# Performance work log

Measured on AMD Instinct MI355X. Metric: run time of the kernel, lower is better.

The kernel has to match this reference:

```python
import jax, jax.numpy as jnp
import numpy as np

BN_EPS = 1e-5


def setup_inputs() -> dict:
    key = jax.random.key(0)
    ks = jax.random.split(key, 10)
    D, N, NDRUG, NTAIL, NREL = 256, 128, 572, 100000, 100
    return {
        "drug_table": jax.random.normal(ks[0], (NDRUG, D), jnp.float32),
        "rela_table": jax.random.normal(ks[1], (NREL, D), jnp.float32),
        "ent_table": jax.random.normal(ks[2], (NTAIL, D), jnp.float32),
        "W1": jax.random.normal(ks[3], (NDRUG, D, D), jnp.float32),
        "b1": jax.random.normal(ks[4], (N, D), jnp.float32),
        "W2": jax.random.normal(ks[5], (NDRUG, D, D), jnp.float32),
        "b2": jax.random.normal(ks[6], (N, D), jnp.float32),
        "lin_w": jax.random.normal(ks[7], (D, 2 * D), jnp.float32) * (1.0 / np.sqrt(2 * D)),
        "lin_b": jnp.zeros((D,), jnp.float32),
        "bn_gamma": jnp.ones((D,), jnp.float32),
        "bn_beta": jnp.zeros((D,), jnp.float32),
        "drug_name": jnp.arange(NDRUG, dtype=jnp.int64) if jax.config.jax_enable_x64 else jnp.arange(NDRUG, dtype=jnp.int32),
        "adj_tail": jax.random.randint(ks[8], (NDRUG, N), 0, NTAIL, jnp.int32),
        "adj_relation": jax.random.randint(ks[9], (NDRUG, N), 0, NREL, jnp.int32),
    }


def reference(drug_table, rela_table, ent_table, W1, b1, W2, b2,
              lin_w, lin_b, bn_gamma, bn_beta,
              drug_name, adj_tail, adj_relation):
    d = drug_table[drug_name]            # (572, D)
    r = rela_table[adj_relation]         # (572, N, D)
    e = ent_table[adj_tail]              # (572, N, D)

    dr = d[:, None, :] * r               # (572, N, D)
    h = jax.nn.relu(jnp.einsum('bnd,bde->bne', dr, W1) + b1)
    h = jnp.einsum('bnd,bde->bne', h, W2) + b2
    score = jax.nn.softmax(jnp.sum(h, axis=-1), axis=1)   # (572, N)
    w_ent = jnp.einsum('bn,bnd->bd', score, e)             # (572, D)

    x = jnp.concatenate([w_ent, d], axis=1)                # (572, 2D)
    y = jax.nn.relu(x @ lin_w.T + lin_b)                   # (572, D)
    # BatchNorm1d in training mode: batch stats, biased variance
    mean = jnp.mean(y, axis=0)
    var = jnp.var(y, axis=0)
    return bn_gamma * (y - mean) * jax.lax.rsqrt(var + BN_EPS) + bn_beta
```

## Files before the change

kernel.cpp:

```cpp
#include <hip/hip_runtime.h>
#include <math.h>

#define DD   256
#define NN   128
#define NB   572
#define NREL 100
#define KS   32
#define NKS  (DD / KS)
#define EH   128
#define RS   80
#define PSS  132
#define LDRUGS 8

typedef _Float16 h8 __attribute__((ext_vector_type(8)));
typedef _Float16 h2 __attribute__((ext_vector_type(2)));
typedef float    f4 __attribute__((ext_vector_type(4)));

__device__ __forceinline__ float4 ld4(const float* p) {
    return *reinterpret_cast<const float4*>(p);
}
__device__ __forceinline__ void split16(float x, _Float16& hi, _Float16& lo) {
    hi = (_Float16)x;
    lo = (_Float16)(x - (float)hi);
}
__device__ __forceinline__ int slotx(int blk2, int row) {
    return ((blk2 ^ (row & 7)) & 7) * 8;
}

__global__ void sum_b2(const float* __restrict__ b2, float* __restrict__ b2s)
{
    const int n = blockIdx.x, t = threadIdx.x;
    float4 v = ld4(&b2[n * DD + t * 4]);
    float s = v.x + v.y + v.z + v.w;
    #pragma unroll
    for (int m = 32; m >= 1; m >>= 1) s += __shfl_xor(s, m, 64);
    if (t == 0) b2s[n] = s;
}

__global__ __launch_bounds__(512, 4)
void gnn_mm(const float* __restrict__ drug_table,
            const float* __restrict__ rela_table,
            const float* __restrict__ W1,
            const float* __restrict__ b1,
            const float* __restrict__ W2,
            const int*   __restrict__ drug_name,
            const int*   __restrict__ adj_relation,
            float* __restrict__ part)
{
    __shared__ __align__(16) _Float16 AB_l[2 * 128 * RS];
    __shared__ float d_l[DD];
    __shared__ float w2s_l[EH];
    __shared__ int   rel_l[NN], urel_l[NN], head_l[NN], next_l[NN];
    __shared__ int   map_l[NREL];
    __shared__ int   U_l, c0_l;

    _Float16* A_l = AB_l;
    _Float16* B_l = AB_l + 128 * RS;
    float*    Pl  = reinterpret_cast<float*>(AB_l);

    const int bid  = blockIdx.x;
    const int b    = bid >> 1, h = bid & 1;
    const int tid  = threadIdx.x;
    const int lane = tid & 63;
    const int wv   = tid >> 6;
    const int rg   = wv >> 2;
    const int cg   = wv & 3;
    const int r16  = lane & 15;
    const int gb   = lane >> 4;

    if (tid < NN) { rel_l[tid] = adj_relation[b * NN + tid]; head_l[tid] = -1; }
    if (tid < NREL) map_l[tid] = -1;
    if (tid < DD)  d_l[tid] = drug_table[(size_t)drug_name[b] * DD + tid];
    __syncthreads();
    if (tid < NN) map_l[rel_l[tid]] = 1;
    __syncthreads();

    bool mk = false; int rank = 0, tot = 0;
    if (tid < 128) {
        mk = (tid < NREL) && (map_l[tid] != -1);
        unsigned long long bal = __ballot(mk);
        rank = __popcll(bal & ((1ull << (tid & 63)) - 1));
        tot  = __popcll(bal);
    }
    if (tid < 64) {
        if (mk) { map_l[tid] = rank; urel_l[rank] = tid; }
        if (tid == 0) c0_l = tot;
    }
    __syncthreads();
    if (tid >= 64 && tid < 128) {
        const int base = c0_l;
        if (mk) { map_l[tid] = base + rank; urel_l[base + rank] = tid; }
        if (tid == 64) U_l = base + tot;
    }
    __syncthreads();
    if (tid < NN)
        next_l[tid] = atomicExch(&head_l[map_l[rel_l[tid]]], tid);
    __syncthreads();

    const int U   = U_l;
    const int NRT = (U + 31) >> 5;

    const float* W1b = W1 + (size_t)b * DD * DD;
    const float* W2b = W2 + (size_t)b * DD * DD;

    {
        const int padrows = NRT * 32 - U;
        h8 z = {(_Float16)0.f,(_Float16)0.f,(_Float16)0.f,(_Float16)0.f,
                (_Float16)0.f,(_Float16)0.f,(_Float16)0.f,(_Float16)0.f};
        for (int x = tid; x < padrows * 8; x += 512) {
            int r = U + (x >> 3), c = (x & 7) * 8;
            *(h8*)&A_l[r * RS + c] = z;
        }
    }

    const int kp  = tid >> 5;
    const int el  = tid & 31;
    const int sau = tid >> 2;
    const int sab = tid & 3;

    float rb0[4], rb1[4];
    float4 raA, raB;

    #define STAGE_LOAD(kt_) {                                                  \
        const int k0_ = (kt_) * KS;                                            \
        const float* w1p0 = &W1b[(size_t)(k0_ + 2 * kp) * DD + h * EH + el];   \
        const float* w1p1 = w1p0 + DD;                                         \
        _Pragma("unroll")                                                      \
        for (int i = 0; i < 4; ++i) {                                          \
            rb0[i] = w1p0[32 * i];                                             \
            rb1[i] = w1p1[32 * i];                                             \
        }                                                                      \
        if (sau < U) {                                                         \
            const float* rr = rela_table + (size_t)urel_l[sau] * DD + k0_ + sab * 8;\
            raA = ld4(rr); raB = ld4(rr + 4);                                  \
        }                                                                      \
    }

    #define STAGE_WRITE(kt_) {                                                 \
        const int k0_ = (kt_) * KS;                                            \
        const float da = d_l[k0_ + 2 * kp], db = d_l[k0_ + 2 * kp + 1];        \
        const int bk2 = 2 * (kp >> 2);                                         \
        const int wo  = (2 * kp) & 7;                                          \
        _Pragma("unroll")                                                      \
        for (int i = 0; i < 4; ++i) {                                          \
            const int e = el + 32 * i;                                         \
            _Float16 h0, l0, h1, l1;                                           \
            split16(rb0[i] * da, h0, l0);                                      \
            split16(rb1[i] * db, h1, l1);                                      \
            h2 th = {h0, h1}, tl = {l0, l1};                                   \
            *(h2*)&B_l[e * RS + slotx(bk2,     e) + wo] = th;                  \
            *(h2*)&B_l[e * RS + slotx(bk2 + 1, e) + wo] = tl;                  \
        }                                                                      \
        if (sau < U) {                                                         \
            const float vr[8] = {raA.x, raA.y, raA.z, raA.w,                   \
                                 raB.x, raB.y, raB.z, raB.w};                  \
            h8 hv, lv;                                                         \
            _Pragma("unroll")                                                  \
            for (int j = 0; j < 8; ++j) {                                      \
                _Float16 hh, ll;                                               \
                split16(vr[j], hh, ll);                                        \
                hv[j] = hh; lv[j] = ll;                                        \
            }                                                                  \
            *(h8*)&A_l[sau * RS + slotx(2 * sab,     sau)] = hv;               \
            *(h8*)&A_l[sau * RS + slotx(2 * sab + 1, sau)] = lv;               \
        }                                                                      \
    }

    STAGE_LOAD(0);
    STAGE_WRITE(0);
    __syncthreads();

    f4 acc[2][2][2];
    #pragma unroll
    for (int p = 0; p < 2; ++p)
        #pragma unroll
        for (int sr = 0; sr < 2; ++sr)
            #pragma unroll
            for (int sc = 0; sc < 2; ++sc)
                acc[p][sr][sc] = {0.f, 0.f, 0.f, 0.f};

    for (int kt = 0; kt < NKS; ++kt) {
        if (kt + 1 < NKS) STAGE_LOAD(kt + 1);

        float4 rw0 = ld4(&W2b[(size_t)(h * EH + kt * 16 + 2 * wv)     * DD + lane * 4]);
        float4 rw1 = ld4(&W2b[(size_t)(h * EH + kt * 16 + 2 * wv + 1) * DD + lane * 4]);

        h8 bh[2], bl[2];
        #pragma unroll
        for (int sc = 0; sc < 2; ++sc) {
            const int e = cg * 32 + sc * 16 + r16;
            bh[sc] = *(const h8*)&B_l[e * RS + slotx(2 * gb,     e)];
            bl[sc] = *(const h8*)&B_l[e * RS + slotx(2 * gb + 1, e)];
        }
        #pragma unroll
        for (int p = 0; p < 2; ++p) {
            const int rt = rg + 2 * p;
            if (rt < NRT) {
                #pragma unroll
                for (int sr = 0; sr < 2; ++sr) {
                    const int row = rt * 32 + sr * 16 + r16;
                    h8 ah = *(const h8*)&A_l[row * RS + slotx(2 * gb,     row)];
                    h8 al = *(const h8*)&A_l[row * RS + slotx(2 * gb + 1, row)];
                    #pragma unroll
                    for (int sc = 0; sc < 2; ++sc) {
                        acc[p][sr][sc] = __builtin_amdgcn_mfma_f32_16x16x32_f16(ah, bh[sc], acc[p][sr][sc], 0, 0, 0);
                        acc[p][sr][sc] = __builtin_amdgcn_mfma_f32_16x16x32_f16(al, bh[sc], acc[p][sr][sc], 0, 0, 0);
                        acc[p][sr][sc] = __builtin_amdgcn_mfma_f32_16x16x32_f16(ah, bl[sc], acc[p][sr][sc], 0, 0, 0);
                    }
                }
            }
        }

        {
            float s0 = rw0.x + rw0.y + rw0.z + rw0.w;
            float s1 = rw1.x + rw1.y + rw1.z + rw1.w;
            #pragma unroll
            for (int m = 32; m >= 1; m >>= 1) {
                s0 += __shfl_xor(s0, m, 64);
                s1 += __shfl_xor(s1, m, 64);
            }
            if (lane == 0) {
                w2s_l[kt * 16 + 2 * wv]     = s0;
                w2s_l[kt * 16 + 2 * wv + 1] = s1;
            }
        }

        __syncthreads();
        if (kt + 1 < NKS) STAGE_WRITE(kt + 1);
        __syncthreads();
    }
    #undef STAGE_LOAD
    #undef STAGE_WRITE

    const int ug   = tid >> 4;
    const int td16 = tid & 15;
    float4 w0 = ld4(&w2s_l[td16 * 8]);
    float4 w1v = ld4(&w2s_l[td16 * 8 + 4]);

    for (int rt = 0; rt < 4; ++rt) {
        if (rt < NRT) {
            __syncthreads();
            if ((rt & 1) == rg) {
                const int p = rt >> 1;
                #pragma unroll
                for (int sr = 0; sr < 2; ++sr)
                    #pragma unroll
                    for (int sc = 0; sc < 2; ++sc)
                        #pragma unroll
                        for (int jj = 0; jj < 4; ++jj)
                            Pl[(sr * 16 + gb * 4 + jj) * PSS + cg * 32 + sc * 16 + r16] =
                                acc[p][sr][sc][jj];
            }
            __syncthreads();
            const int u = rt * 32 + ug;
            if (u < U) {
                float4 p0 = ld4(&Pl[ug * PSS + td16 * 8]);
                float4 p1 = ld4(&Pl[ug * PSS + td16 * 8 + 4]);
                int n = head_l[u];
                while (n >= 0) {
                    const float* bp = b1 + (size_t)n * DD + h * EH + td16 * 8;
                    float4 b0 = ld4(bp);
                    float4 b1v = ld4(bp + 4);
                    float s = fmaxf(p0.x + b0.x,  0.f) * w0.x
                            + fmaxf(p0.y + b0.y,  0.f) * w0.y
                            + fmaxf(p0.z + b0.z,  0.f) * w0.z
                            + fmaxf(p0.w + b0.w,  0.f) * w0.w
                            + fmaxf(p1.x + b1v.x, 0.f) * w1v.x
                            + fmaxf(p1.y + b1v.y, 0.f) * w1v.y
                            + fmaxf(p1.z + b1v.z, 0.f) * w1v.z
                            + fmaxf(p1.w + b1v.w, 0.f) * w1v.w;
                    #pragma unroll
                    for (int m = 8; m >= 1; m >>= 1) s += __shfl_xor(s, m, 16);
                    if (td16 == 0) part[(size_t)b * 256 + h * NN + n] = s;
                    n = next_l[n];
                }
            }
        }
    }
}

__global__ __launch_bounds__(256)
void gnn_gather(const float* __restrict__ drug_table,
                const float* __restrict__ ent_table,
                const int*   __restrict__ drug_name,
                const int*   __restrict__ adj_tail,
                const float* __restrict__ part,
                const float* __restrict__ b2s_g,
                float* __restrict__ xbuf)
{
    __shared__ float score_l[NN];
    __shared__ int   tail_l[NN];

    const int b = blockIdx.x, tid = threadIdx.x;

    if (tid < NN) {
        tail_l[tid]  = adj_tail[b * NN + tid];
        score_l[tid] = part[(size_t)b * 256 + tid]
                     + part[(size_t)b * 256 + NN + tid] + b2s_g[tid];
    }
    __syncthreads();

    if (tid < 64) {
        float l0 = score_l[tid], l1 = score_l[tid + 64];
        float M = fmaxf(l0, l1);
        #pragma unroll
        for (int m = 32; m >= 1; m >>= 1) M = fmaxf(M, __shfl_xor(M, m, 64));
        float e0 = expf(l0 - M), e1 = expf(l1 - M);
        float S = e0 + e1;
        #pragma unroll
        for (int m = 32; m >= 1; m >>= 1) S += __shfl_xor(S, m, 64);
        float inv = 1.f / S;
        score_l[tid]      = e0 * inv;
        score_l[tid + 64] = e1 * inv;
    }
    __syncthreads();

    float w = 0.f;
    for (int n = 0; n < NN; ++n) {
        float s = score_l[n];
        if (s > 1e-9f)
            w = fmaf(s, ent_table[(size_t)tail_l[n] * DD + tid], w);
    }
    xbuf[(size_t)b * 512 + tid]       = w;
    xbuf[(size_t)b * 512 + 256 + tid] = drug_table[(size_t)drug_name[b] * DD + tid];
}

__global__ __launch_bounds__(256)
void gnn_lin(const float* __restrict__ lin_w,
             const float* __restrict__ lin_b,
             const float* __restrict__ xbuf,
             float* __restrict__ Y)
{
    __shared__ float x_l[LDRUGS * 512];

    const int g = blockIdx.x, tid = threadIdx.x;
    const int b0 = g * LDRUGS;

    #pragma unroll
    for (int i = 0; i < LDRUGS * 2; ++i) {
        int f = tid + i * 256;
        *reinterpret_cast<float4*>(&x_l[f * 4]) = ld4(&xbuf[(size_t)b0 * 512 + f * 4]);
    }
    __syncthreads();

    const float* lw = lin_w + (size_t)tid * 512;
    float dot[LDRUGS];
    #pragma unroll
    for (int d = 0; d < LDRUGS; ++d) dot[d] = 0.f;

    for (int k4 = 0; k4 < 128; ++k4) {
        float4 wv = ld4(&lw[k4 * 4]);
        #pragma unroll
        for (int d = 0; d < LDRUGS; ++d) {
            float4 xv = ld4(&x_l[d * 512 + k4 * 4]);
            dot[d] += wv.x * xv.x + wv.y * xv.y + wv.z * xv.z + wv.w * xv.w;
        }
    }

    const float bb = lin_b[tid];
    #pragma unroll
    for (int d = 0; d < LDRUGS; ++d) {
        if (b0 + d < NB)
            Y[(size_t)(b0 + d) * DD + tid] = fmaxf(dot[d] + bb, 0.f);
    }
}

__global__ void bn_stats(const float* __restrict__ Y, float* __restrict__ stats)
{
    int d = blockIdx.x, t = threadIdx.x;
    float s = 0.f, ss = 0.f;
    for (int b = t; b < NB; b += 64) {
        float v = Y[(size_t)b * DD + d];
        s += v; ss += v * v;
    }
    #pragma unroll
    for (int m = 32; m >= 1; m >>= 1) {
        s  += __shfl_xor(s, m, 64);
        ss += __shfl_xor(ss, m, 64);
    }
    if (t == 0) {
        float mean = s * (1.f / NB);
        float var  = ss * (1.f / NB) - mean * mean;
        stats[d]      = mean;
        stats[DD + d] = rsqrtf(var + 1e-5f);
    }
}

__global__ void bn_apply(float* __restrict__ Y, const float* __restrict__ stats,
                         const float* __restrict__ gamma, const float* __restrict__ beta)
{
    int b = blockIdx.x, t = threadIdx.x;
    float mean = stats[t], inv = stats[DD + t];
    float v = Y[(size_t)b * DD + t];
    Y[(size_t)b * DD + t] = gamma[t] * (v - mean) * inv + beta[t];
}

extern "C" void kernel_launch(void* const* d_in, const int* in_sizes, int n_in,
                              void* d_out, int out_size, void* d_ws, size_t ws_size,
                              hipStream_t stream)
{
    const float* drug_table = (const float*)d_in[0];
    const float* rela_table = (const float*)d_in[1];
    const float* ent_table  = (const float*)d_in[2];
    const float* W1         = (const float*)d_in[3];
    const float* b1         = (const float*)d_in[4];
    const float* W2         = (const float*)d_in[5];
    const float* b2         = (const float*)d_in[6];
    const float* lin_w      = (const float*)d_in[7];
    const float* lin_b      = (const float*)d_in[8];
    const float* bn_g       = (const float*)d_in[9];
    const float* bn_b       = (const float*)d_in[10];
    const int*   drug_name  = (const int*)d_in[11];
    const int*   adj_tail   = (const int*)d_in[12];
    const int*   adj_rel    = (const int*)d_in[13];
    float* out = (float*)d_out;

    const int NBP = ((NB + LDRUGS - 1) / LDRUGS) * LDRUGS;
    float* b2s   = (float*)d_ws;
    float* part  = b2s + NN;
    float* xbuf  = part + (size_t)NB * 256;
    float* stats = xbuf + (size_t)NBP * 512;

    sum_b2<<<NN, 64, 0, stream>>>(b2, b2s);
    gnn_mm<<<2 * NB, 512, 0, stream>>>(drug_table, rela_table, W1, b1, W2,
                                       drug_name, adj_rel, part);
    gnn_gather<<<NB, 256, 0, stream>>>(drug_table, ent_table, drug_name,
                                       adj_tail, part, b2s, xbuf);
    gnn_lin<<<NBP / LDRUGS, 256, 0, stream>>>(lin_w, lin_b, xbuf, out);
    bn_stats<<<DD, 64, 0, stream>>>(out, stats);
    bn_apply<<<NB, DD, 0, stream>>>(out, stats, bn_g, bn_b);
}
```

Baseline: 130.4 us.

## Add dedicated producer waves for W2 row sums and vectorize W1 staging

The gnn_mm block grows from 8 to 10 waves. The two extra waves only load W2 rows and reduce them into the w2s shared buffer, while the original 8 waves do the W1/rela staging and the MFMA split-fp16 GEMM, so the W2 traffic overlaps with the matrix work instead of sitting in the compute waves. W1 staging is remapped so each thread loads 8 consecutive k rows for one output column and writes whole h8 vectors to LDS instead of h2 pairs. The launch bounds change to (640, 8), which may squeeze registers and cause spills, and the extra waves add scheduling pressure at every block barrier.

```diff
diff --git a/kernel.cpp b/kernel.cpp
--- a/kernel.cpp
+++ b/kernel.cpp
@@ -10,6 +10,7 @@
 #define EH   128
 #define RS   80
 #define PSS  132
+#define NT   640
 #define LDRUGS 8
 
 typedef _Float16 h8 __attribute__((ext_vector_type(8)));
@@ -37,7 +38,7 @@
     if (t == 0) b2s[n] = s;
 }
 
-__global__ __launch_bounds__(512, 4)
+__global__ __launch_bounds__(NT, 8)
 void gnn_mm(const float* __restrict__ drug_table,
             const float* __restrict__ rela_table,
             const float* __restrict__ W1,
@@ -107,68 +108,57 @@
         const int padrows = NRT * 32 - U;
         h8 z = {(_Float16)0.f,(_Float16)0.f,(_Float16)0.f,(_Float16)0.f,
                 (_Float16)0.f,(_Float16)0.f,(_Float16)0.f,(_Float16)0.f};
-        for (int x = tid; x < padrows * 8; x += 512) {
+        for (int x = tid; x < padrows * 8; x += NT) {
             int r = U + (x >> 3), c = (x & 7) * 8;
             *(h8*)&A_l[r * RS + c] = z;
         }
     }
 
-    const int kp  = tid >> 5;
-    const int el  = tid & 31;
+    const int kb  = (tid >> 7) & 3;
+    const int be  = tid & 127;
     const int sau = tid >> 2;
     const int sab = tid & 3;
 
-    float rb0[4], rb1[4];
+    float rbv[8];
     float4 raA, raB;
 
     #define STAGE_LOAD(kt_) {                                                  \
-        const int k0_ = (kt_) * KS;                                            \
-        const float* w1p0 = &W1b[(size_t)(k0_ + 2 * kp) * DD + h * EH + el];   \
-        const float* w1p1 = w1p0 + DD;                                         \
+        const int k0_ = (kt_) * KS + kb * 8;                                   \
+        const float* wp = &W1b[(size_t)k0_ * DD + h * EH + be];                \
         _Pragma("unroll")                                                      \
-        for (int i = 0; i < 4; ++i) {                                          \
-            rb0[i] = w1p0[32 * i];                                             \
-            rb1[i] = w1p1[32 * i];                                             \
-        }                                                                      \
+        for (int j = 0; j < 8; ++j) rbv[j] = wp[(size_t)j * DD];               \
         if (sau < U) {                                                         \
-            const float* rr = rela_table + (size_t)urel_l[sau] * DD + k0_ + sab * 8;\
+            const float* rr = rela_table + (size_t)urel_l[sau] * DD            \
+                              + (kt_) * KS + sab * 8;                          \
             raA = ld4(rr); raB = ld4(rr + 4);                                  \
         }                                                                      \
     }
 
     #define STAGE_WRITE(kt_) {                                                 \
-        const int k0_ = (kt_) * KS;                                            \
-        const float da = d_l[k0_ + 2 * kp], db = d_l[k0_ + 2 * kp + 1];        \
-        const int bk2 = 2 * (kp >> 2);                                         \
-        const int wo  = (2 * kp) & 7;                                          \
+        const int k0_ = (kt_) * KS + kb * 8;                                   \
+        h8 hv, lv;                                                             \
         _Pragma("unroll")                                                      \
-        for (int i = 0; i < 4; ++i) {                                          \
-            const int e = el + 32 * i;                                         \
-            _Float16 h0, l0, h1, l1;                                           \
-            split16(rb0[i] * da, h0, l0);                                      \
-            split16(rb1[i] * db, h1, l1);                                      \
-            h2 th = {h0, h1}, tl = {l0, l1};                                   \
-            *(h2*)&B_l[e * RS + slotx(bk2,     e) + wo] = th;                  \
-            *(h2*)&B_l[e * RS + slotx(bk2 + 1, e) + wo] = tl;                  \
+        for (int j = 0; j < 8; ++j) {                                          \
+            _Float16 hh, ll;                                                   \
+            split16(rbv[j] * d_l[k0_ + j], hh, ll);                            \
+            hv[j] = hh; lv[j] = ll;                                            \
         }                                                                      \
+        *(h8*)&B_l[be * RS + slotx(2 * kb,     be)] = hv;                      \
+        *(h8*)&B_l[be * RS + slotx(2 * kb + 1, be)] = lv;                      \
         if (sau < U) {                                                         \
             const float vr[8] = {raA.x, raA.y, raA.z, raA.w,                   \
                                  raB.x, raB.y, raB.z, raB.w};                  \
-            h8 hv, lv;                                                         \
+            h8 ahv, alv;                                                       \
             _Pragma("unroll")                                                  \
             for (int j = 0; j < 8; ++j) {                                      \
                 _Float16 hh, ll;                                               \
                 split16(vr[j], hh, ll);                                        \
-                hv[j] = hh; lv[j] = ll;                                        \
+                ahv[j] = hh; alv[j] = ll;                                      \
             }                                                                  \
-            *(h8*)&A_l[sau * RS + slotx(2 * sab,     sau)] = hv;               \
-            *(h8*)&A_l[sau * RS + slotx(2 * sab + 1, sau)] = lv;               \
+            *(h8*)&A_l[sau * RS + slotx(2 * sab,     sau)] = ahv;              \
+            *(h8*)&A_l[sau * RS + slotx(2 * sab + 1, sau)] = alv;              \
         }                                                                      \
     }
-
-    STAGE_LOAD(0);
-    STAGE_WRITE(0);
-    __syncthreads();
 
     f4 acc[2][2][2];
     #pragma unroll
@@ -179,54 +169,56 @@
             for (int sc = 0; sc < 2; ++sc)
                 acc[p][sr][sc] = {0.f, 0.f, 0.f, 0.f};
 
+    if (wv < 8) { STAGE_LOAD(0); }
+    __syncthreads();
+    if (wv < 8) { STAGE_WRITE(0); }
+    __syncthreads();
+
     for (int kt = 0; kt < NKS; ++kt) {
-        if (kt + 1 < NKS) STAGE_LOAD(kt + 1);
-
-        float4 rw0 = ld4(&W2b[(size_t)(h * EH + kt * 16 + 2 * wv)     * DD + lane * 4]);
-        float4 rw1 = ld4(&W2b[(size_t)(h * EH + kt * 16 + 2 * wv + 1) * DD + lane * 4]);
-
-        h8 bh[2], bl[2];
-        #pragma unroll
-        for (int sc = 0; sc < 2; ++sc) {
-            const int e = cg * 32 + sc * 16 + r16;
-            bh[sc] = *(const h8*)&B_l[e * RS + slotx(2 * gb,     e)];
-            bl[sc] = *(const h8*)&B_l[e * RS + slotx(2 * gb + 1, e)];
-        }
-        #pragma unroll
-        for (int p = 0; p < 2; ++p) {
-            const int rt = rg + 2 * p;
-            if (rt < NRT) {
-                #pragma unroll
-                for (int sr = 0; sr < 2; ++sr) {
-                    const int row = rt * 32 + sr * 16 + r16;
-                    h8 ah = *(const h8*)&A_l[row * RS + slotx(2 * gb,     row)];
-                    h8 al = *(const h8*)&A_l[row * RS + slotx(2 * gb + 1, row)];
+        if (wv < 8) {
+            if (kt + 1 < NKS) STAGE_LOAD(kt + 1);
+
+            h8 bh[2], bl[2];
+            #pragma unroll
+            for (int sc = 0; sc < 2; ++sc) {
+                const int e = cg * 32 + sc * 16 + r16;
+                bh[sc] = *(const h8*)&B_l[e * RS + slotx(2 * gb,     e)];
+                bl[sc] = *(const h8*)&B_l[e * RS + slotx(2 * gb + 1, e)];
+            }
+            #pragma unroll
+            for (int p = 0; p < 2; ++p) {
+                const int rt = rg + 2 * p;
+                if (rt < NRT) {
                     #pragma unroll
-                    for (int sc = 0; sc < 2; ++sc) {
-                        acc[p][sr][sc] = __builtin_amdgcn_mfma_f32_16x16x32_f16(ah, bh[sc], acc[p][sr][sc], 0, 0, 0);
-                        acc[p][sr][sc] = __builtin_amdgcn_mfma_f32_16x16x32_f16(al, bh[sc], acc[p][sr][sc], 0, 0, 0);
-                        acc[p][sr][sc] = __builtin_amdgcn_mfma_f32_16x16x32_f16(ah, bl[sc], acc[p][sr][sc], 0, 0, 0);
+                    for (int sr = 0; sr < 2; ++sr) {
+                        const int row = rt * 32 + sr * 16 + r16;
+                        h8 ah = *(const h8*)&A_l[row * RS + slotx(2 * gb,     row)];
+                        h8 al = *(const h8*)&A_l[row * RS + slotx(2 * gb + 1, row)];
+                        #pragma unroll
+                        for (int sc = 0; sc < 2; ++sc) {
+                            acc[p][sr][sc] = __builtin_amdgcn_mfma_f32_16x16x32_f16(ah, bh[sc], acc[p][sr][sc], 0, 0, 0);
+                            acc[p][sr][sc] = __builtin_amdgcn_mfma_f32_16x16x32_f16(al, bh[sc], acc[p][sr][sc], 0, 0, 0);
+                            acc[p][sr][sc] = __builtin_amdgcn_mfma_f32_16x16x32_f16(ah, bl[sc], acc[p][sr][sc], 0, 0, 0);
+                        }
                     }
                 }
             }
-        }
-
-        {
-            float s0 = rw0.x + rw0.y + rw0.z + rw0.w;
-            float s1 = rw1.x + rw1.y + rw1.z + rw1.w;
+        } else {
+            const int r0 = (wv - 8) * 64 + kt * 8;
+            float4 rv[8];
             #pragma unroll
-            for (int m = 32; m >= 1; m >>= 1) {
-                s0 += __shfl_xor(s0, m, 64);
-                s1 += __shfl_xor(s1, m, 64);
-            }
-            if (lane == 0) {
-                w2s_l[kt * 16 + 2 * wv]     = s0;
-                w2s_l[kt * 16 + 2 * wv + 1] = s1;
+            for (int j = 0; j < 8; ++j)
+                rv[j] = ld4(&W2b[(size_t)(h * EH + r0 + j) * DD + lane * 4]);
+            #pragma unroll
+            for (int j = 0; j < 8; ++j) {
+                float s = rv[j].x + rv[j].y + rv[j].z + rv[j].w;
+                #pragma unroll
+                for (int m = 32; m >= 1; m >>= 1) s += __shfl_xor(s, m, 64);
+                if (lane == 0) w2s_l[r0 + j] = s;
             }
         }
-
         __syncthreads();
-        if (kt + 1 < NKS) STAGE_WRITE(kt + 1);
+        if (wv < 8 && kt + 1 < NKS) STAGE_WRITE(kt + 1);
         __syncthreads();
     }
     #undef STAGE_LOAD
@@ -240,7 +232,7 @@
     for (int rt = 0; rt < 4; ++rt) {
         if (rt < NRT) {
             __syncthreads();
-            if ((rt & 1) == rg) {
+            if (wv < 8 && (rt & 1) == rg) {
                 const int p = rt >> 1;
                 #pragma unroll
                 for (int sr = 0; sr < 2; ++sr)
@@ -253,7 +245,7 @@
             }
             __syncthreads();
             const int u = rt * 32 + ug;
-            if (u < U) {
+            if (ug < 32 && u < U) {
                 float4 p0 = ld4(&Pl[ug * PSS + td16 * 8]);
                 float4 p1 = ld4(&Pl[ug * PSS + td16 * 8 + 4]);
                 int n = head_l[u];
@@ -422,8 +414,8 @@
     float* stats = xbuf + (size_t)NBP * 512;
 
     sum_b2<<<NN, 64, 0, stream>>>(b2, b2s);
-    gnn_mm<<<2 * NB, 512, 0, stream>>>(drug_table, rela_table, W1, b1, W2,
-                                       drug_name, adj_rel, part);
+    gnn_mm<<<2 * NB, NT, 0, stream>>>(drug_table, rela_table, W1, b1, W2,
+                                      drug_name, adj_rel, part);
     gnn_gather<<<NB, 256, 0, stream>>>(drug_table, ent_table, drug_name,
                                        adj_tail, part, b2s, xbuf);
     gnn_lin<<<NBP / LDRUGS, 256, 0, stream>>>(lin_w, lin_b, xbuf, out);
```

New measurement: 345.9 us. 165% more time.
